# Performance work log

Hardware: AMD Instinct MI355X
Metric: run time of the kernel (lower is better)

Reference implementation:

```python
import jax, jax.numpy as jnp
import numpy as np

# dims: H heads, D=word_size (d_model), E=embed_dim per head, N=seq_len=n, K=linformer k
H, D, E, N, K = 16, 1024, 64, 4096, 256


def setup_inputs() -> dict:
    key = jax.random.key(0)
    ks = jax.random.split(key, 9)
    s = 0.02  # init scale for weights
    return {
        "x":  jax.random.normal(ks[0], (N, D), jnp.float32),
        # per-head QKV linears: torch Linear weight is (out=E, in=D), bias (E,)
        "Wq": jax.random.normal(ks[1], (H, E, D), jnp.float32) * s,
        "bq": jnp.zeros((H, E), jnp.float32),
        "Wk": jax.random.normal(ks[2], (H, E, D), jnp.float32) * s,
        "bk": jnp.zeros((H, E), jnp.float32),
        "Wv": jax.random.normal(ks[3], (H, E, D), jnp.float32) * s,
        "bv": jnp.zeros((H, E), jnp.float32),
        # per-head E/F sequence projections: Linear(n=N, k=K) -> weight (K, N), bias (K,)
        "Ew": jax.random.normal(ks[4], (H, K, N), jnp.float32) * s,
        "Eb": jnp.zeros((H, K), jnp.float32),
        "Fw": jax.random.normal(ks[5], (H, K, N), jnp.float32) * s,
        "Fb": jnp.zeros((H, K), jnp.float32),
        # output projection: Linear(H*E, E, bias=False) -> weight (E, H*E)
        "Wo": jax.random.normal(ks[6], (E, H * E), jnp.float32) * s,
    }


def reference(x, Wq, bq, Wk, bk, Wv, bv, Ew, Eb, Fw, Fb, Wo):
    # per-head Q/K/V projections, batched over heads: (H, N, E)
    q = jnp.einsum('nd,hed->hne', x, Wq) + bq[:, None, :]
    k = jnp.einsum('nd,hed->hne', x, Wk) + bk[:, None, :]
    v = jnp.einsum('nd,hed->hne', x, Wv) + bv[:, None, :]
    # low-rank sequence-length projection of K and V: (H, K, E)
    kp = jnp.einsum('hjn,hne->hje', Ew, k) + Eb[:, :, None]
    vp = jnp.einsum('hjn,hne->hje', Fw, v) + Fb[:, :, None]
    # scaled dot-product attention against projected keys: (H, N, K)
    score = jnp.einsum('hne,hje->hnj', q, kp) / jnp.sqrt(jnp.float32(E))
    attn = jax.nn.softmax(score, axis=-1)
    z = jnp.einsum('hnj,hje->hne', attn, vp)  # (H, N, E)
    # concat heads along feature dim (matches torch.cat(dim=1)): (N, H*E)
    zs = jnp.transpose(z, (1, 0, 2)).reshape(N, H * E)
    # final projection Linear(H*E, E, bias=False)
    return zs @ Wo.T  # (N, E)
```

## Files before the change

kernel.cpp:

```cpp
#include <hip/hip_runtime.h>
#include <hip/hip_bf16.h>

typedef __attribute__((ext_vector_type(4))) float f32x4;
typedef __attribute__((ext_vector_type(8))) short s16x8;
typedef __attribute__((ext_vector_type(4))) short s16x4;
typedef unsigned short u16;


__device__ __forceinline__ f32x4 mfma16(s16x8 a, s16x8 b, f32x4 c) {
    return __builtin_amdgcn_mfma_f32_16x16x32_bf16(a, b, c, 0, 0, 0);
}

__device__ __forceinline__ u16 bf(float f) {
    union { float f; unsigned u; } x; x.f = f;
    return (u16)((x.u + 0x7fffu + ((x.u >> 16) & 1u)) >> 16);
}
__device__ __forceinline__ unsigned pkbf(float a, float b) {
    union { float f; unsigned u; } x, y; x.f = a; y.f = b;
    unsigned ra = x.u + 0x7fffu + ((x.u >> 16) & 1u);
    unsigned rb = y.u + 0x7fffu + ((y.u >> 16) & 1u);
    return (ra >> 16) | (rb & 0xffff0000u);
}

__device__ __forceinline__ void gl_lds16(const void* g, void* l) {
    __builtin_amdgcn_global_load_lds(
        (const __attribute__((address_space(1))) unsigned*)g,
        (__attribute__((address_space(3))) unsigned*)l, 16, 0, 0);
}


__global__ __launch_bounds__(256) void cvt_all_kernel(
        const float* __restrict__ x,  const float* __restrict__ Wq,
        const float* __restrict__ Wk, const float* __restrict__ Wv,
        const float* __restrict__ Wo,
        u16* __restrict__ xb, u16* __restrict__ wb, u16* __restrict__ wob) {
    int i = blockIdx.x * 256 + threadIdx.x;
    const float* src; u16* dst; int off;
    if (i < 1048576)      { src = x;  dst = xb;            off = i; }
    else if (i < 1310720) { src = Wq; dst = wb;            off = i - 1048576; }
    else if (i < 1572864) { src = Wk; dst = wb + 1048576;  off = i - 1310720; }
    else if (i < 1835008) { src = Wv; dst = wb + 2097152;  off = i - 1572864; }
    else if (i < 1851392) { src = Wo; dst = wob;           off = i - 1835008; }
    else return;
    f32x4 v = ((const f32x4*)src)[off];
    union { s16x4 v; unsigned u[2]; } r;
    r.u[0] = pkbf(v.x, v.y);
    r.u[1] = pkbf(v.z, v.w);
    ((s16x4*)dst)[off] = r.v;
}


__global__ __launch_bounds__(256, 3) void qkv_kernel(
        const u16* __restrict__ xb, const u16* __restrict__ wb,
        const float* __restrict__ bq, const float* __restrict__ bk,
        const float* __restrict__ bv,
        u16* __restrict__ qo, u16* __restrict__ kTo, u16* __restrict__ vTo) {
    __shared__ u16 As[128 * 32];
    __shared__ u16 Bs[128 * 32];
    int bx   = blockIdx.x % 24;
    int by   = blockIdx.x / 24;
    int tid  = threadIdx.x;
    int lane = tid & 63, w = tid >> 6;
    int l15  = lane & 15, quad = lane >> 4;
    int wr   = w >> 1, wc = w & 1;

    const u16* Ag = xb + (size_t)(by * 128 + (tid >> 2)) * 1024 + (tid & 3) * 8;
    const u16* Bg = wb + (size_t)(bx * 128 + (tid >> 2)) * 1024 + (tid & 3) * 8;
    u16* Al = As + tid * 8;
    u16* Bl = Bs + tid * 8;

    const u16* abase = As + (wr * 64 + l15) * 32 + quad * 8;
    const u16* bbase = Bs + (wc * 64 + l15) * 32 + quad * 8;

    f32x4 acc[4][4] = {};
    for (int k0 = 0; k0 < 1024; k0 += 32) {
        gl_lds16(Ag + k0, Al);
        gl_lds16(Ag + 64 * 1024 + k0, Al + 64 * 32);
        gl_lds16(Bg + k0, Bl);
        gl_lds16(Bg + 64 * 1024 + k0, Bl + 64 * 32);
        __syncthreads();
        s16x8 a[4], b[4];
#pragma unroll
        for (int mi = 0; mi < 4; mi++) a[mi] = *(const s16x8*)(abase + mi * 16 * 32);
#pragma unroll
        for (int nj = 0; nj < 4; nj++) b[nj] = *(const s16x8*)(bbase + nj * 16 * 32);
#pragma unroll
        for (int mi = 0; mi < 4; mi++)
#pragma unroll
            for (int nj = 0; nj < 4; nj++) acc[mi][nj] = mfma16(a[mi], b[nj], acc[mi][nj]);
        __syncthreads();
    }

    int fblk = (bx * 128 + wc * 64) >> 6;
    int mat  = fblk >> 4, h = fblk & 15;
    const float* bias = (mat == 0) ? bq : (mat == 1 ? bk : bv);
#pragma unroll
    for (int nj = 0; nj < 4; nj++) {
        int e = nj * 16 + l15;
        float bb = bias[h * 64 + e];
#pragma unroll
        for (int mi = 0; mi < 4; mi++) {
            int n0 = by * 128 + wr * 64 + mi * 16 + quad * 4;
            f32x4 c = acc[mi][nj];
            if (mat == 0) {
                u16* p = qo + ((size_t)h * 4096 + n0) * 64 + e;
#pragma unroll
                for (int r = 0; r < 4; r++) p[(size_t)r * 64] = bf(c[r] + bb);
            } else {
                u16* p = (mat == 1 ? kTo : vTo) + ((size_t)h * 64 + e) * 4096 + n0;
                union { s16x4 v; u16 s[4]; } pk;
#pragma unroll
                for (int r = 0; r < 4; r++) pk.s[r] = bf(c[r] + bb);
                *(s16x4*)p = pk.v;
            }
        }
    }
}


__global__ __launch_bounds__(512, 2) void kpvp_kernel(
        const float* __restrict__ Ew, const float* __restrict__ Fw,
        const u16* __restrict__ kT, const u16* __restrict__ vT,
        float* __restrict__ accs) {
    __shared__ u16 Als[64 * 256];
    __shared__ u16 Bls[64 * 256];
    int b   = blockIdx.x;
    int ks  = b & 1, jb = (b >> 1) & 3, h = (b >> 3) & 15, p = b >> 7;
    int tid = threadIdx.x;
    int w = tid >> 6, lane = tid & 63;
    int l15 = lane & 15, quad = lane >> 4;
    int wm = w >> 2, we = w & 3;

    const float* Abase = (p ? Fw : Ew)
        + (size_t)(h * 256 + jb * 64) * 4096 + ks * 2048;
    const char* Bbase = (const char*)(p ? vT : kT)
        + (size_t)h * 64 * 8192 + ks * 4096;

    f32x4 areg[8];
#pragma unroll
    for (int pr = 0; pr < 8; pr++)
        areg[pr] = *(const f32x4*)(Abase + (size_t)(pr * 8 + w) * 4096 + lane * 4);

    f32x4 acc[2] = {};

#pragma unroll
    for (int s = 0; s < 8; s++) {
        __syncthreads();
#pragma unroll
        for (int i = 0; i < 4; i++) {
            int row = (w * 4 + i) * 2 + (lane >> 5);
            int c   = lane & 31;
            int cg  = (c & 24) | ((c & 7) ^ (row & 7));
            gl_lds16(Bbase + (size_t)row * 8192 + s * 512 + cg * 16,
                     (char*)Bls + (w * 4 + i) * 1024);
        }
#pragma unroll
        for (int pr = 0; pr < 8; pr++) {
            int row = pr * 8 + w;
            union { s16x4 q; unsigned u[2]; } rr;
            rr.u[0] = pkbf(areg[pr].x, areg[pr].y);
            rr.u[1] = pkbf(areg[pr].z, areg[pr].w);
            int c  = lane >> 1;
            int cw = (c & 24) | ((c & 7) ^ (w & 7));
            *(s16x4*)((char*)Als + row * 512 + cw * 16 + (lane & 1) * 8) = rr.q;
        }
        __syncthreads();
        if (s < 7) {
#pragma unroll
            for (int pr = 0; pr < 8; pr++)
                areg[pr] = *(const f32x4*)(Abase + (size_t)(pr * 8 + w) * 4096
                                           + (s + 1) * 256 + lane * 4);
        }
#pragma unroll
        for (int t = 0; t < 8; t++) {
            int c  = 4 * t + quad;
            int ca = (c & 24) | ((c & 7) ^ (l15 & 7));
            s16x8 bv = *(const s16x8*)((char*)Bls + (we * 16 + l15) * 512 + ca * 16);
            s16x8 a0 = *(const s16x8*)((char*)Als + (wm * 32 + l15) * 512 + ca * 16);
            s16x8 a1 = *(const s16x8*)((char*)Als + (wm * 32 + 16 + l15) * 512 + ca * 16);
            acc[0] = mfma16(a0, bv, acc[0]);
            acc[1] = mfma16(a1, bv, acc[1]);
        }
    }

    size_t obase = (size_t)ks * 524288 + ((size_t)(p * 16 + h) * 256 + jb * 64) * 64;
#pragma unroll
    for (int mt = 0; mt < 2; mt++)
#pragma unroll
        for (int r = 0; r < 4; r++) {
            int jrow = wm * 32 + mt * 16 + quad * 4 + r;
            accs[obase + (size_t)jrow * 64 + we * 16 + l15] = acc[mt][r];
        }
}


__global__ __launch_bounds__(256) void packkv_kernel(
        const float* __restrict__ accs, const float* __restrict__ Eb,
        const float* __restrict__ Fb, u16* __restrict__ kp, u16* __restrict__ vpT) {
    int idx = blockIdx.x * 256 + threadIdx.x;
    float v = accs[idx] + accs[idx + 524288];
    int p = idx >> 18, h = (idx >> 14) & 15, j = (idx >> 6) & 255, e = idx & 63;
    if (p == 0) {
        v += Eb[h * 256 + j];
        kp[((size_t)(h * 256 + j)) * 64 + e] = bf(v * 0.125f);
    } else {
        v += Fb[h * 256 + j];
        vpT[((size_t)(h * 64 + e)) * 256 + j] = bf(v);
    }
}


__global__ __launch_bounds__(256, 2) void attn_kernel(
        const u16* __restrict__ q, const u16* __restrict__ kp,
        const u16* __restrict__ vpT, u16* __restrict__ zs) {
    __shared__ u16 kv[16384];
    __shared__ u16 ps[4][16][256];
    int bm   = blockIdx.x & 63, h = blockIdx.x >> 6;
    int tid  = threadIdx.x;
    int lane = tid & 63, w = tid >> 6;
    int l15  = lane & 15, quad = lane >> 4;
    int nbase = bm * 64 + w * 16;

    {
        int r8 = lane >> 3;
        int cg = (lane & 7) ^ r8;
        const u16* src = kp + (size_t)h * 16384;
#pragma unroll
        for (int it = 0; it < 8; it++) {
            int row = it * 32 + w * 8 + r8;
            gl_lds16(src + row * 64 + cg * 8, (char*)kv + it * 4096 + w * 1024);
        }
    }
    const u16* qp = q + ((size_t)h * 4096 + nbase + l15) * 64 + quad * 8;
    s16x8 qa0 = *(const s16x8*)(qp);
    s16x8 qa1 = *(const s16x8*)(qp + 32);
    __syncthreads();

    f32x4 s[16] = {};
#pragma unroll
    for (int jt = 0; jt < 16; jt++) {
        int c0 = quad ^ (l15 & 7);
        int c1 = (quad + 4) ^ (l15 & 7);
        const char* rowp = (const char*)kv + (jt * 16 + l15) * 128;
        s16x8 b0 = *(const s16x8*)(rowp + c0 * 16);
        s16x8 b1 = *(const s16x8*)(rowp + c1 * 16);
        s[jt] = mfma16(qa0, b0, s[jt]);
        s[jt] = mfma16(qa1, b1, s[jt]);
    }

    float lsum[4];
#pragma unroll
    for (int r = 0; r < 4; r++) {
        float m = s[0][r];
#pragma unroll
        for (int jt = 1; jt < 16; jt++) m = fmaxf(m, s[jt][r]);
        m = fmaxf(m, __shfl_xor(m, 1));
        m = fmaxf(m, __shfl_xor(m, 2));
        m = fmaxf(m, __shfl_xor(m, 4));
        m = fmaxf(m, __shfl_xor(m, 8));
        float l = 0.f;
#pragma unroll
        for (int jt = 0; jt < 16; jt++) {
            float pv = __expf(s[jt][r] - m);
            s[jt][r] = pv;
            l += pv;
        }
        l += __shfl_xor(l, 1);
        l += __shfl_xor(l, 2);
        l += __shfl_xor(l, 4);
        l += __shfl_xor(l, 8);
        lsum[r] = l;
    }

    __syncthreads();
    {
        int r2 = lane >> 5;
        int c  = lane & 31;
        const u16* src = vpT + (size_t)h * 16384;
#pragma unroll
        for (int it = 0; it < 8; it++) {
            int row = it * 8 + w * 2 + r2;
            int cg  = (c & 24) | ((c & 7) ^ (row & 7));
            gl_lds16(src + row * 256 + cg * 8, (char*)kv + it * 4096 + w * 1024);
        }
    }
#pragma unroll
    for (int jt = 0; jt < 16; jt++)
#pragma unroll
        for (int r = 0; r < 4; r++) {
            int row = quad * 4 + r;
            ps[w][row][(jt * 16 + l15) ^ ((row & 7) << 3)] = bf(s[jt][r]);
        }
    __syncthreads();

    f32x4 z[4] = {};
#pragma unroll
    for (int kj = 0; kj < 8; kj++) {
        s16x8 a = *(const s16x8*)&ps[w][l15][(kj * 32 + quad * 8) ^ ((l15 & 7) << 3)];
#pragma unroll
        for (int et = 0; et < 4; et++) {
            int c  = kj * 4 + quad;
            int cs = (c & 24) | ((c & 7) ^ (l15 & 7));
            s16x8 bv = *(const s16x8*)((char*)kv + (et * 16 + l15) * 512 + cs * 16);
            z[et] = mfma16(a, bv, z[et]);
        }
    }
#pragma unroll
    for (int et = 0; et < 4; et++) {
        int e = et * 16 + l15;
        u16* o = zs + ((size_t)(nbase + quad * 4)) * 1024 + h * 64 + e;
#pragma unroll
        for (int r = 0; r < 4; r++) o[(size_t)r * 1024] = bf(z[et][r] / lsum[r]);
    }
}


__global__ __launch_bounds__(256) void out_kernel(
        const u16* __restrict__ zs, const u16* __restrict__ wob,
        float* __restrict__ oslice) {
    int ks   = blockIdx.x & 3;
    int bm   = blockIdx.x >> 2;
    int lane = threadIdx.x & 63, w = threadIdx.x >> 6;
    int l15  = lane & 15, quad = lane >> 4;
    int row0 = bm * 128 + w * 32;

    const u16* A = zs  + (size_t)(row0 + l15) * 1024 + ks * 256 + quad * 8;
    const u16* B = wob + (size_t)l15 * 1024 + ks * 256 + quad * 8;

    f32x4 acc[2][4] = {};
    for (int k = 0; k < 256; k += 32) {
        s16x8 a0 = *(const s16x8*)(A + k);
        s16x8 a1 = *(const s16x8*)(A + 16 * 1024 + k);
#pragma unroll
        for (int nt = 0; nt < 4; nt++) {
            s16x8 bv = *(const s16x8*)(B + (size_t)nt * 16 * 1024 + k);
            acc[0][nt] = mfma16(a0, bv, acc[0][nt]);
            acc[1][nt] = mfma16(a1, bv, acc[1][nt]);
        }
    }
    float* os = oslice + (size_t)ks * 262144;
#pragma unroll
    for (int mt = 0; mt < 2; mt++)
#pragma unroll
        for (int nt = 0; nt < 4; nt++) {
            int e = nt * 16 + l15;
            int n0 = row0 + mt * 16 + quad * 4;
            float* o = os + (size_t)n0 * 64 + e;
#pragma unroll
            for (int r = 0; r < 4; r++) o[(size_t)r * 64] = acc[mt][nt][r];
        }
}

__global__ __launch_bounds__(256) void outred_kernel(
        const float* __restrict__ oslice, float* __restrict__ out) {
    int i = blockIdx.x * 256 + threadIdx.x;
    out[i] = oslice[i] + oslice[i + 262144] + oslice[i + 524288] + oslice[i + 786432];
}


extern "C" void kernel_launch(void* const* d_in, const int* in_sizes, int n_in,
                              void* d_out, int out_size, void* d_ws, size_t ws_size,
                              hipStream_t stream) {
    const float* x  = (const float*)d_in[0];
    const float* Wq = (const float*)d_in[1];
    const float* bq = (const float*)d_in[2];
    const float* Wk = (const float*)d_in[3];
    const float* bk = (const float*)d_in[4];
    const float* Wv = (const float*)d_in[5];
    const float* bv = (const float*)d_in[6];
    const float* Ew = (const float*)d_in[7];
    const float* Eb = (const float*)d_in[8];
    const float* Fw = (const float*)d_in[9];
    const float* Fb = (const float*)d_in[10];
    const float* Wo = (const float*)d_in[11];

    char* ws = (char*)d_ws;
    u16*   qb   = (u16*)(ws + 0);
    u16*   kT   = (u16*)(ws + 8388608);
    u16*   vT   = (u16*)(ws + 16777216);
    u16*   zsb  = (u16*)(ws + 25165824);
    float* accs = (float*)(ws + 33554432);
    u16*   kp   = (u16*)(ws + 67108864);
    u16*   vpT  = (u16*)(ws + 67633152);
    u16*   xb   = (u16*)(ws + 68157440);
    u16*   wb   = (u16*)(ws + 76546048);
    u16*   wob  = (u16*)(ws + 82837504);

    cvt_all_kernel<<<7232, 256, 0, stream>>>(x, Wq, Wk, Wv, Wo, xb, wb, wob);
    qkv_kernel<<<768, 256, 0, stream>>>(xb, wb, bq, bk, bv, qb, kT, vT);
    kpvp_kernel<<<256, 512, 0, stream>>>(Ew, Fw, kT, vT, accs);
    packkv_kernel<<<2048, 256, 0, stream>>>(accs, Eb, Fb, kp, vpT);
    attn_kernel<<<1024, 256, 0, stream>>>(qb, kp, vpT, zsb);
    out_kernel<<<128, 256, 0, stream>>>(zsb, wob, (float*)accs);
    outred_kernel<<<1024, 256, 0, stream>>>((const float*)accs, (float*)d_out);
}
```

Before: 264.2 us.

## Double-buffer LDS tiles in kpvp kernel with one barrier per step

The E/F sequence-projection GEMM kernel now keeps two LDS buffers for the A and B tiles. Each iteration fills the next buffer (bf16 convert of A, async global-to-LDS copy of B) and issues global loads two stages ahead, while MFMAs run on the current buffer. This replaces the two __syncthreads per stage with one barrier and explicit waitcnt and sched_barrier control, so load latency can overlap compute. The cost is twice the LDS per block, which may stop two 512-thread blocks fitting on one CU, and the hand-placed waitcnts are fragile.

```diff
diff --git a/kernel.cpp b/kernel.cpp
--- a/kernel.cpp
+++ b/kernel.cpp
@@ -122,8 +122,8 @@
         const float* __restrict__ Ew, const float* __restrict__ Fw,
         const u16* __restrict__ kT, const u16* __restrict__ vT,
         float* __restrict__ accs) {
-    __shared__ u16 Als[64 * 256];
-    __shared__ u16 Bls[64 * 256];
+    __shared__ u16 Als[2][64 * 256];
+    __shared__ u16 Bls[2][64 * 256];
     int b   = blockIdx.x;
     int ks  = b & 1, jb = (b >> 1) & 3, h = (b >> 3) & 15, p = b >> 7;
     int tid = threadIdx.x;
@@ -137,51 +137,84 @@
         + (size_t)h * 64 * 8192 + ks * 4096;
 
     f32x4 areg[8];
-#pragma unroll
-    for (int pr = 0; pr < 8; pr++)
-        areg[pr] = *(const f32x4*)(Abase + (size_t)(pr * 8 + w) * 4096 + lane * 4);
+
+#define LOAD_A(s)                                                          \
+    _Pragma("unroll")                                                      \
+    for (int pr = 0; pr < 8; pr++)                                         \
+        areg[pr] = *(const f32x4*)(Abase + (size_t)(pr * 8 + w) * 4096     \
+                                   + (s) * 256 + lane * 4);
+
+#define WRITE_A(s)                                                         \
+    {                                                                      \
+        char* dst = (char*)Als[(s) & 1];                                   \
+        _Pragma("unroll")                                                  \
+        for (int pr = 0; pr < 8; pr++) {                                   \
+            int row = pr * 8 + w;                                          \
+            union { s16x4 q; unsigned u[2]; } rr;                          \
+            rr.u[0] = pkbf(areg[pr].x, areg[pr].y);                        \
+            rr.u[1] = pkbf(areg[pr].z, areg[pr].w);                        \
+            int c  = lane >> 1;                                            \
+            int cw = (c & 24) | ((c & 7) ^ (w & 7));                       \
+            *(s16x4*)(dst + row * 512 + cw * 16 + (lane & 1) * 8) = rr.q;  \
+        }                                                                  \
+    }
+
+#define STAGE_B(s)                                                         \
+    {                                                                      \
+        char* dst = (char*)Bls[(s) & 1];                                   \
+        _Pragma("unroll")                                                  \
+        for (int i = 0; i < 4; i++) {                                      \
+            int row = (w * 4 + i) * 2 + (lane >> 5);                       \
+            int c   = lane & 31;                                           \
+            int cg  = (c & 24) | ((c & 7) ^ (row & 7));                    \
+            gl_lds16(Bbase + (size_t)row * 8192 + (s) * 512 + cg * 16,     \
+                     dst + (w * 4 + i) * 1024);                            \
+        }                                                                  \
+    }
+
+    LOAD_A(0);
+    asm volatile("s_waitcnt vmcnt(0)" ::: "memory");
+    WRITE_A(0);
+    STAGE_B(0);
+    __builtin_amdgcn_sched_barrier(0);
+    LOAD_A(1);
+    __builtin_amdgcn_sched_barrier(0);
+    asm volatile("s_waitcnt lgkmcnt(0)" ::: "memory");
 
     f32x4 acc[2] = {};
-
 #pragma unroll
     for (int s = 0; s < 8; s++) {
-        __syncthreads();
-#pragma unroll
-        for (int i = 0; i < 4; i++) {
-            int row = (w * 4 + i) * 2 + (lane >> 5);
-            int c   = lane & 31;
-            int cg  = (c & 24) | ((c & 7) ^ (row & 7));
-            gl_lds16(Bbase + (size_t)row * 8192 + s * 512 + cg * 16,
-                     (char*)Bls + (w * 4 + i) * 1024);
-        }
-#pragma unroll
-        for (int pr = 0; pr < 8; pr++) {
-            int row = pr * 8 + w;
-            union { s16x4 q; unsigned u[2]; } rr;
-            rr.u[0] = pkbf(areg[pr].x, areg[pr].y);
-            rr.u[1] = pkbf(areg[pr].z, areg[pr].w);
-            int c  = lane >> 1;
-            int cw = (c & 24) | ((c & 7) ^ (w & 7));
-            *(s16x4*)((char*)Als + row * 512 + cw * 16 + (lane & 1) * 8) = rr.q;
-        }
-        __syncthreads();
+        if (s < 7) asm volatile("s_waitcnt vmcnt(8)" ::: "memory");
+        else       asm volatile("s_waitcnt vmcnt(0)" ::: "memory");
+        __builtin_amdgcn_s_barrier();
+        __builtin_amdgcn_sched_barrier(0);
         if (s < 7) {
-#pragma unroll
-            for (int pr = 0; pr < 8; pr++)
-                areg[pr] = *(const f32x4*)(Abase + (size_t)(pr * 8 + w) * 4096
-                                           + (s + 1) * 256 + lane * 4);
-        }
+            asm volatile("s_waitcnt vmcnt(0)" ::: "memory");
+            WRITE_A(s + 1);
+            STAGE_B(s + 1);
+            __builtin_amdgcn_sched_barrier(0);
+        }
+        if (s < 6) {
+            LOAD_A(s + 2);
+            __builtin_amdgcn_sched_barrier(0);
+        }
+        const char* ab  = (const char*)Als[s & 1];
+        const char* bbf = (const char*)Bls[s & 1];
 #pragma unroll
         for (int t = 0; t < 8; t++) {
             int c  = 4 * t + quad;
             int ca = (c & 24) | ((c & 7) ^ (l15 & 7));
-            s16x8 bv = *(const s16x8*)((char*)Bls + (we * 16 + l15) * 512 + ca * 16);
-            s16x8 a0 = *(const s16x8*)((char*)Als + (wm * 32 + l15) * 512 + ca * 16);
-            s16x8 a1 = *(const s16x8*)((char*)Als + (wm * 32 + 16 + l15) * 512 + ca * 16);
+            s16x8 bv = *(const s16x8*)(bbf + (we * 16 + l15) * 512 + ca * 16);
+            s16x8 a0 = *(const s16x8*)(ab + (wm * 32 + l15) * 512 + ca * 16);
+            s16x8 a1 = *(const s16x8*)(ab + (wm * 32 + 16 + l15) * 512 + ca * 16);
             acc[0] = mfma16(a0, bv, acc[0]);
             acc[1] = mfma16(a1, bv, acc[1]);
         }
-    }
+        asm volatile("s_waitcnt lgkmcnt(0)" ::: "memory");
+    }
+#undef LOAD_A
+#undef WRITE_A
+#undef STAGE_B
 
     size_t obase = (size_t)ks * 524288 + ((size_t)(p * 16 + h) * 256 + jb * 64) * 64;
 #pragma unroll
```

Result: no change. 265.6 us (+0.5%).
